# Kernel tuning notes

Hardware: AMD Instinct MI355X
Metric: run time of the kernel (lower is better)

## Reference

```python
import jax, jax.numpy as jnp
import numpy as np

N_ATOM = 10000
N_EDGE = 40000
D = 64          # fingerprint_dim
BOND_DIM = 10
EPS_BN = 1e-6
EPS_SM = 1e-8


def _bn(x, g, b, m, v):
    # BatchNorm1d in eval mode with running stats
    return (x - m) * jax.lax.rsqrt(v + EPS_BN) * g + b


def setup_inputs() -> dict:
    key = jax.random.key(0)
    ks = jax.random.split(key, 16)
    s = 0.05
    inp = {
        "atom": jax.random.normal(ks[0], (N_ATOM, D), jnp.float32),
        "bond_index": jax.random.randint(ks[1], (N_EDGE, 2), 0, N_ATOM, jnp.int64),
        "bond": jax.random.normal(ks[2], (N_EDGE, BOND_DIM), jnp.float32),
        # encoder: Linear(bond_dim, D*D) + BN(D*D)
        "enc_W": jax.random.normal(ks[3], (D * D, BOND_DIM), jnp.float32) * s,
        "enc_b": jnp.zeros((D * D,), jnp.float32),
        "bn1_g": jnp.ones((D * D,), jnp.float32),
        "bn1_b": jnp.zeros((D * D,), jnp.float32),
        "bn1_m": jnp.zeros((D * D,), jnp.float32),
        "bn1_v": jnp.ones((D * D,), jnp.float32),
        # align: Linear(2D, 1)
        "align_W": jax.random.normal(ks[4], (1, 2 * D), jnp.float32) * s,
        "align_b": jnp.zeros((1,), jnp.float32),
        # attend: Linear(D, D) + BN(D)
        "att_W": jax.random.normal(ks[5], (D, D), jnp.float32) * s,
        "att_b": jnp.zeros((D,), jnp.float32),
        "bn2_g": jnp.ones((D,), jnp.float32),
        "bn2_b": jnp.zeros((D,), jnp.float32),
        "bn2_m": jnp.zeros((D,), jnp.float32),
        "bn2_v": jnp.ones((D,), jnp.float32),
        # GRUCell(D, D)
        "gru_Wih": jax.random.normal(ks[6], (3 * D, D), jnp.float32) * s,
        "gru_Whh": jax.random.normal(ks[7], (3 * D, D), jnp.float32) * s,
        "gru_bih": jnp.zeros((3 * D,), jnp.float32),
        "gru_bhh": jnp.zeros((3 * D,), jnp.float32),
    }
    return inp


def reference(atom, bond_index, bond, enc_W, enc_b, bn1_g, bn1_b, bn1_m, bn1_v,
              align_W, align_b, att_W, att_b, bn2_g, bn2_b, bn2_m, bn2_v,
              gru_Wih, gru_Whh, gru_bih, gru_bhh):
    num_atom, atom_dim = atom.shape
    tgt = bond_index[:, 0]  # segment index (bond_index.t()[0])
    nbr = bond_index[:, 1]

    # encoder: Linear + BN + ReLU, then view as per-edge [D, D] matrices
    enc = jax.nn.relu(_bn(bond @ enc_W.T + enc_b, bn1_g, bn1_b, bn1_m, bn1_v))
    enc = enc.reshape(-1, atom_dim, atom_dim)            # [E, D, D]

    neighbor = jnp.einsum('ed,edf->ef', atom[nbr], enc)  # per-edge bmm [E, D]
    target_atom = atom[tgt]

    feat = jnp.concatenate([target_atom, neighbor], axis=-1)       # [E, 2D]
    align_score = jax.nn.leaky_relu(feat @ align_W.T + align_b)    # [E, 1]

    atend = _bn(neighbor @ att_W.T + att_b, bn2_g, bn2_b, bn2_m, bn2_v)  # [E, D]

    # segment softmax over edges grouped by target atom
    seg_max = jax.ops.segment_max(align_score, tgt, num_segments=num_atom)
    ex = jnp.exp(align_score - seg_max[tgt])
    denom = jax.ops.segment_sum(ex, tgt, num_segments=num_atom)[tgt] + EPS_SM
    w = ex / denom                                                   # [E, 1]

    context = jax.ops.segment_sum(w * atend, tgt, num_segments=num_atom)  # [N, D]
    context = jax.nn.elu(context)

    # GRUCell(context, atom)
    gi = context @ gru_Wih.T + gru_bih
    gh = atom @ gru_Whh.T + gru_bhh
    i_r, i_z, i_n = jnp.split(gi, 3, axis=-1)
    h_r, h_z, h_n = jnp.split(gh, 3, axis=-1)
    r = jax.nn.sigmoid(i_r + h_r)
    z = jax.nn.sigmoid(i_z + h_z)
    n = jnp.tanh(i_n + r * h_n)
    update = (1.0 - z) * n + z * atom
    return update
```

## Files before the change

kernel.cpp:

```cpp
#include <hip/hip_runtime.h>

#define N_ATOM 10000
#define N_EDGE 40000
#define DD 64
#define BOND_DIM 10
#define EPS_BN 1e-6f
#define EPS_SM 1e-8f
#define GA 8

typedef __attribute__((ext_vector_type(8))) short short8;
typedef __attribute__((ext_vector_type(2))) float float2v;
typedef __attribute__((ext_vector_type(4))) float float4v;
typedef __attribute__((ext_vector_type(16))) float float16v;
typedef unsigned int u32;

constexpr size_t OFF_AFRAG   = 0;
constexpr size_t OFF_ATTFRAG = 32768;
constexpr size_t OFF_ATTB    = 34816;
constexpr size_t OFF_WIHT    = 34880;
constexpr size_t OFF_WHHT    = 47168;
constexpr size_t OFF_DENOM   = 59456;
constexpr size_t OFF_CTX     = 69456;

__device__ __forceinline__ unsigned short f2bf(float x) {
    u32 u = __float_as_uint(x);
    u32 r = u + 0x7FFFu + ((u >> 16) & 1u);
    return (unsigned short)(r >> 16);
}

__global__ void fold_kernel(const float* enc_W, const float* enc_b,
                            const float* g1, const float* b1,
                            const float* m1, const float* v1,
                            const float* att_W, const float* att_b,
                            const float* g2, const float* b2v,
                            const float* m2, const float* v2,
                            const float* Wih, const float* Whh,
                            float* ws) {
    u32* wsu = (u32*)ws;
    size_t i = (size_t)blockIdx.x * 256 + threadIdx.x;
    if (i < 8192) {
        int d = i >> 7, rem = i & 127;
        int ch = rem >> 6, l = rem & 63;
        int c = d * 64 + ch * 32 + (l & 31);
        int kb = 8 * (l >> 5);
        float s = g1[c] * rsqrtf(v1[c] + EPS_BN);
        float bias = enc_b[c] * s + b1[c] - m1[c] * s;
        unsigned short h[8];
#pragma unroll
        for (int j = 0; j < 8; j++) {
            int k = kb + j;
            float v = (k < BOND_DIM) ? enc_W[c * BOND_DIM + k] * s
                                     : ((k == BOND_DIM) ? bias : 0.f);
            h[j] = f2bf(v);
        }
#pragma unroll
        for (int m = 0; m < 4; m++)
            wsu[OFF_AFRAG + i * 4 + m] = (u32)h[2 * m] | ((u32)h[2 * m + 1] << 16);
    } else if (i < 8704) {
        int idx = i - 8192;
        int l = idx & 63, fckh = idx >> 6;
        int fc = fckh >> 1, kh = fckh & 1, q = l >> 4;
        int n = (fc << 4) + (l & 15);
        float s = g2[n] * rsqrtf(v2[n] + EPS_BN);
        unsigned short h[8];
#pragma unroll
        for (int j = 0; j < 8; j++) {
            int k = 32 * kh + 8 * q + j;
            h[j] = f2bf(att_W[n * DD + k] * s);
        }
#pragma unroll
        for (int m = 0; m < 4; m++)
            wsu[OFF_ATTFRAG + (size_t)idx * 4 + m] = (u32)h[2 * m] | ((u32)h[2 * m + 1] << 16);
    } else if (i < 8768) {
        int f = i - 8704;
        float s = g2[f] * rsqrtf(v2[f] + EPS_BN);
        ws[OFF_ATTB + f] = att_b[f] * s + b2v[f] - m2[f] * s;
    } else if (i < 21056) {
        int j = i - 8768;
        int d = j / 192, t = j % 192;
        ws[OFF_WIHT + j] = Wih[t * DD + d];
    } else if (i < 33344) {
        int j = i - 21056;
        int d = j / 192, t = j % 192;
        ws[OFF_WHHT + j] = Whh[t * DD + d];
    } else {
        size_t z = i - 33344;
        if (z < (size_t)N_ATOM + (size_t)N_ATOM * DD) ws[OFF_DENOM + z] = 0.f;
    }
}

__global__ __launch_bounds__(256, 5) void edge_kernel(
    const float* atom, const int* bidx, const float* bond,
    const float* alignW, const float* alignb,
    const float* ws, float* denom, float* ctx) {
    __shared__ float s_bond[32][BOND_DIM];
    __shared__ float s_anbr[32][65];
    __shared__ float s_nbp[2][32][65];
    __shared__ float s_ex[32];
    __shared__ int   s_tgt[32];

    const int t = threadIdx.x;
    const int lane = t & 63;
    const int h = t >> 6;
    const int e0 = blockIdx.x * 32;

    for (int idx = t; idx < 32 * BOND_DIM; idx += 256)
        s_bond[idx / BOND_DIM][idx % BOND_DIM] = bond[(size_t)e0 * BOND_DIM + idx];
    if (t < 32) s_tgt[t] = bidx[2 * (e0 + t)];
    for (int e = h; e < 32; e += 4) {
        int nbr = bidx[2 * (e0 + e) + 1];
        s_anbr[e][lane] = atom[(size_t)nbr * DD + lane];
    }
    __syncthreads();

    const int eb = lane & 31;
    const int kb = 8 * (lane >> 5);
    short8 bfrag;
#pragma unroll
    for (int j = 0; j < 8; j++) {
        int k = kb + j;
        unsigned short hh = 0;
        if (k < BOND_DIM) hh = f2bf(s_bond[eb][k]);
        else if (k == BOND_DIM) hh = 0x3F80u;
        bfrag[j] = (short)hh;
    }

    const short8* afrag = (const short8*)((const u32*)ws + OFF_AFRAG);
    const float16v zero16 = {};
    const float2v zero2 = {0.f, 0.f};
    float2v nb0[8] = {}, nb1[8] = {};
    const int d0 = 16 * h;
    const int ph = blockIdx.x & 15;

#pragma unroll
    for (int it = 0; it < 16; it++) {
        int d = d0 + ((it + ph) & 15);
        short8 a0 = afrag[(size_t)(d * 2 + 0) * 64 + lane];
        short8 a1 = afrag[(size_t)(d * 2 + 1) * 64 + lane];
        float av = s_anbr[eb][d];
        float2v av2 = {av, av};
        float16v enc0 = __builtin_amdgcn_mfma_f32_32x32x16_bf16(a0, bfrag, zero16, 0, 0, 0);
        float16v enc1 = __builtin_amdgcn_mfma_f32_32x32x16_bf16(a1, bfrag, zero16, 0, 0, 0);
#pragma unroll
        for (int r = 0; r < 8; r++) {
            float2v e0v = {enc0[2 * r], enc0[2 * r + 1]};
            float2v e1v = {enc1[2 * r], enc1[2 * r + 1]};
            e0v = __builtin_elementwise_max(e0v, zero2);
            e1v = __builtin_elementwise_max(e1v, zero2);
            nb0[r] += av2 * e0v;
            nb1[r] += av2 * e1v;
        }
    }

    const int fro = 4 * (lane >> 5);
    if (h < 2) {
#pragma unroll
        for (int r = 0; r < 8; r++) {
            int e = 2 * r;
            int f = (e & 3) + 8 * (e >> 2) + fro;
            s_nbp[h][eb][f] = nb0[r].x;
            s_nbp[h][eb][f + 1] = nb0[r].y;
            s_nbp[h][eb][32 + f] = nb1[r].x;
            s_nbp[h][eb][32 + f + 1] = nb1[r].y;
        }
    }
    __syncthreads();
    if (h >= 2) {
#pragma unroll
        for (int r = 0; r < 8; r++) {
            int e = 2 * r;
            int f = (e & 3) + 8 * (e >> 2) + fro;
            s_nbp[h - 2][eb][f] += nb0[r].x;
            s_nbp[h - 2][eb][f + 1] += nb0[r].y;
            s_nbp[h - 2][eb][32 + f] += nb1[r].x;
            s_nbp[h - 2][eb][32 + f + 1] += nb1[r].y;
        }
    }
    __syncthreads();

    const int es = (h & 1) * 16;
    const int q = lane >> 4;
    const int r16 = lane & 15;
    float4v att[4];

    if (h < 2) {
        short8 na[2];
#pragma unroll
        for (int kh = 0; kh < 2; kh++)
#pragma unroll
            for (int j = 0; j < 8; j++) {
                int k = 32 * kh + 8 * q + j;
                na[kh][j] = (short)f2bf(s_nbp[0][es + r16][k] + s_nbp[1][es + r16][k]);
            }
        const short8* battfrag = (const short8*)((const u32*)ws + OFF_ATTFRAG);
        const float4v zero4 = {0.f, 0.f, 0.f, 0.f};
#pragma unroll
        for (int fc = 0; fc < 4; fc++) {
            att[fc] = __builtin_amdgcn_mfma_f32_16x16x32_bf16(na[0], battfrag[(fc * 2 + 0) * 64 + lane], zero4, 0, 0, 0);
            att[fc] = __builtin_amdgcn_mfma_f32_16x16x32_bf16(na[1], battfrag[(fc * 2 + 1) * 64 + lane], att[fc], 0, 0, 0);
            float ab = ws[OFF_ATTB + fc * 16 + r16];
#pragma unroll
            for (int r = 0; r < 4; r++) att[fc][r] += ab;
        }
    } else {
        const float aw1 = alignW[lane];
        const float aw2 = alignW[64 + lane];
        const float alb = alignb[0];
#pragma unroll 4
        for (int e = 0; e < 16; e++) {
            int le = es + e;
            int tgt = s_tgt[le];
            float nbv = s_nbp[0][le][lane] + s_nbp[1][le][lane];
            float v = atom[(size_t)tgt * DD + lane] * aw1 + nbv * aw2;
#pragma unroll
            for (int off = 32; off > 0; off >>= 1) v += __shfl_xor(v, off);
            float sc = v + alb;
            sc = sc > 0.f ? sc : 0.01f * sc;
            float ex = expf(sc);
            if (lane == 0) {
                s_ex[le] = ex;
                atomicAdd(&denom[tgt], ex);
            }
        }
    }
    __syncthreads();

    if (h < 2) {
#pragma unroll
        for (int r = 0; r < 4; r++) {
            int le = es + 4 * q + r;
            float exr = s_ex[le];
            int tg = s_tgt[le];
#pragma unroll
            for (int fc = 0; fc < 4; fc++)
                atomicAdd(&ctx[(size_t)tg * DD + fc * 16 + r16], exr * att[fc][r]);
        }
    }
}

__global__ __launch_bounds__(192) void gru_kernel(
    const float* atom, const float* ws, const float* denom, const float* ctx,
    const float* bih, const float* bhh, float* out) {
    __shared__ float sctx[GA][DD];
    __shared__ float satom[GA][DD];
    __shared__ float sgi[GA][192];
    __shared__ float sgh[GA][192];
    const int a0 = blockIdx.x * GA;
    const int t = threadIdx.x;

    for (int idx = t; idx < GA * DD; idx += 192) {
        int a = idx >> 6, f = idx & 63;
        float c = ctx[(size_t)(a0 + a) * DD + f] / (denom[a0 + a] + EPS_SM);
        sctx[a][f] = c > 0.f ? c : expm1f(c);
        satom[a][f] = atom[(size_t)(a0 + a) * DD + f];
    }
    __syncthreads();

    const float* wiht = ws + OFF_WIHT;
    const float* whht = ws + OFF_WHHT;
    float gi[GA], gh[GA];
    const float bi = bih[t], bh = bhh[t];
#pragma unroll
    for (int a = 0; a < GA; a++) { gi[a] = bi; gh[a] = bh; }
#pragma unroll 4
    for (int d = 0; d < DD; d++) {
        float wi = wiht[d * 192 + t];
        float wh = whht[d * 192 + t];
#pragma unroll
        for (int a = 0; a < GA; a++) {
            gi[a] = fmaf(wi, sctx[a][d], gi[a]);
            gh[a] = fmaf(wh, satom[a][d], gh[a]);
        }
    }
#pragma unroll
    for (int a = 0; a < GA; a++) { sgi[a][t] = gi[a]; sgh[a][t] = gh[a]; }
    __syncthreads();

    for (int idx = t; idx < GA * DD; idx += 192) {
        int a = idx >> 6, f = idx & 63;
        float r = 1.f / (1.f + expf(-(sgi[a][f] + sgh[a][f])));
        float z = 1.f / (1.f + expf(-(sgi[a][64 + f] + sgh[a][64 + f])));
        float n = tanhf(sgi[a][128 + f] + r * sgh[a][128 + f]);
        out[(size_t)(a0 + a) * DD + f] = (1.f - z) * n + z * satom[a][f];
    }
}

extern "C" void kernel_launch(void* const* d_in, const int* in_sizes, int n_in,
                              void* d_out, int out_size, void* d_ws, size_t ws_size,
                              hipStream_t stream) {
    const float* atom   = (const float*)d_in[0];
    const int*   bidx   = (const int*)d_in[1];
    const float* bond   = (const float*)d_in[2];
    const float* enc_W  = (const float*)d_in[3];
    const float* enc_b  = (const float*)d_in[4];
    const float* bn1_g  = (const float*)d_in[5];
    const float* bn1_b  = (const float*)d_in[6];
    const float* bn1_m  = (const float*)d_in[7];
    const float* bn1_v  = (const float*)d_in[8];
    const float* alignW = (const float*)d_in[9];
    const float* alignb = (const float*)d_in[10];
    const float* att_W  = (const float*)d_in[11];
    const float* att_b  = (const float*)d_in[12];
    const float* bn2_g  = (const float*)d_in[13];
    const float* bn2_b  = (const float*)d_in[14];
    const float* bn2_m  = (const float*)d_in[15];
    const float* bn2_v  = (const float*)d_in[16];
    const float* gWih   = (const float*)d_in[17];
    const float* gWhh   = (const float*)d_in[18];
    const float* gbih   = (const float*)d_in[19];
    const float* gbhh   = (const float*)d_in[20];

    float* ws  = (float*)d_ws;
    float* out = (float*)d_out;

    fold_kernel<<<2670, 256, 0, stream>>>(enc_W, enc_b, bn1_g, bn1_b, bn1_m, bn1_v,
                                          att_W, att_b, bn2_g, bn2_b, bn2_m, bn2_v,
                                          gWih, gWhh, ws);

    edge_kernel<<<N_EDGE / 32, 256, 0, stream>>>(
        atom, bidx, bond, alignW, alignb, ws,
        ws + OFF_DENOM, ws + OFF_CTX);

    gru_kernel<<<N_ATOM / GA, 192, 0, stream>>>(atom, ws, ws + OFF_DENOM, ws + OFF_CTX,
                                                gbih, gbhh, out);
}
```

Measured before the change: 147.5 us.

## Precompute per-atom target align score and drop rotated weight-fragment indexing

Adds a per-atom precomputation in the fold kernel of the target half of the align dot product (atom · alignW[:64]), stored in the workspace. The edge kernel then reads one scalar per edge instead of gathering a 64-float target atom row and doing the multiply. It also removes the per-block phase rotation of the d loop so weight fragment addresses become compile-time offsets, and lowers the edge kernel's min-blocks-per-SM launch bound from 5 to 4. The tradeoffs are extra fold-kernel work over all atoms, possibly more cache-bank contention on the shared weight fragments without the rotation, and occupancy changes from the relaxed bound.

```diff
diff --git a/kernel.cpp b/kernel.cpp
--- a/kernel.cpp
+++ b/kernel.cpp
@@ -19,8 +19,9 @@
 constexpr size_t OFF_ATTB    = 34816;
 constexpr size_t OFF_WIHT    = 34880;
 constexpr size_t OFF_WHHT    = 47168;
-constexpr size_t OFF_DENOM   = 59456;
-constexpr size_t OFF_CTX     = 69456;
+constexpr size_t OFF_SALIGN  = 59456;
+constexpr size_t OFF_DENOM   = 69456;
+constexpr size_t OFF_CTX     = 79456;
 
 __device__ __forceinline__ unsigned short f2bf(float x) {
     u32 u = __float_as_uint(x);
@@ -28,7 +29,8 @@
     return (unsigned short)(r >> 16);
 }
 
-__global__ void fold_kernel(const float* enc_W, const float* enc_b,
+__global__ void fold_kernel(const float* atom, const float* alignW,
+                            const float* enc_W, const float* enc_b,
                             const float* g1, const float* b1,
                             const float* m1, const float* v1,
                             const float* att_W, const float* att_b,
@@ -83,13 +85,24 @@
         int j = i - 21056;
         int d = j / 192, t = j % 192;
         ws[OFF_WHHT + j] = Whh[t * DD + d];
+    } else if (i < 43344) {
+        int a = i - 33344;
+        const float4* ar = (const float4*)(atom + (size_t)a * DD);
+        const float4* aw = (const float4*)alignW;
+        float s = 0.f;
+#pragma unroll
+        for (int qq = 0; qq < 16; qq++) {
+            float4 x = ar[qq], w = aw[qq];
+            s += x.x * w.x + x.y * w.y + x.z * w.z + x.w * w.w;
+        }
+        ws[OFF_SALIGN + a] = s;
     } else {
-        size_t z = i - 33344;
+        size_t z = i - 43344;
         if (z < (size_t)N_ATOM + (size_t)N_ATOM * DD) ws[OFF_DENOM + z] = 0.f;
     }
 }
 
-__global__ __launch_bounds__(256, 5) void edge_kernel(
+__global__ __launch_bounds__(256, 4) void edge_kernel(
     const float* atom, const int* bidx, const float* bond,
     const float* alignW, const float* alignb,
     const float* ws, float* denom, float* ctx) {
@@ -125,19 +138,17 @@
         bfrag[j] = (short)hh;
     }
 
-    const short8* afrag = (const short8*)((const u32*)ws + OFF_AFRAG);
+    const int d0 = 16 * h;
+    const short8* aw = (const short8*)((const u32*)ws + OFF_AFRAG) + ((size_t)(d0 * 2) * 64 + lane);
     const float16v zero16 = {};
     const float2v zero2 = {0.f, 0.f};
     float2v nb0[8] = {}, nb1[8] = {};
-    const int d0 = 16 * h;
-    const int ph = blockIdx.x & 15;
 
 #pragma unroll
     for (int it = 0; it < 16; it++) {
-        int d = d0 + ((it + ph) & 15);
-        short8 a0 = afrag[(size_t)(d * 2 + 0) * 64 + lane];
-        short8 a1 = afrag[(size_t)(d * 2 + 1) * 64 + lane];
-        float av = s_anbr[eb][d];
+        short8 a0 = aw[(size_t)(2 * it) * 64];
+        short8 a1 = aw[(size_t)(2 * it + 1) * 64];
+        float av = s_anbr[eb][d0 + it];
         float2v av2 = {av, av};
         float16v enc0 = __builtin_amdgcn_mfma_f32_32x32x16_bf16(a0, bfrag, zero16, 0, 0, 0);
         float16v enc1 = __builtin_amdgcn_mfma_f32_32x32x16_bf16(a1, bfrag, zero16, 0, 0, 0);
@@ -203,18 +214,17 @@
             for (int r = 0; r < 4; r++) att[fc][r] += ab;
         }
     } else {
-        const float aw1 = alignW[lane];
+        const float* salign = ws + OFF_SALIGN;
         const float aw2 = alignW[64 + lane];
         const float alb = alignb[0];
 #pragma unroll 4
         for (int e = 0; e < 16; e++) {
             int le = es + e;
             int tgt = s_tgt[le];
-            float nbv = s_nbp[0][le][lane] + s_nbp[1][le][lane];
-            float v = atom[(size_t)tgt * DD + lane] * aw1 + nbv * aw2;
+            float v = (s_nbp[0][le][lane] + s_nbp[1][le][lane]) * aw2;
 #pragma unroll
             for (int off = 32; off > 0; off >>= 1) v += __shfl_xor(v, off);
-            float sc = v + alb;
+            float sc = salign[tgt] + v + alb;
             sc = sc > 0.f ? sc : 0.01f * sc;
             float ex = expf(sc);
             if (lane == 0) {
@@ -313,7 +323,8 @@
     float* ws  = (float*)d_ws;
     float* out = (float*)d_out;
 
-    fold_kernel<<<2670, 256, 0, stream>>>(enc_W, enc_b, bn1_g, bn1_b, bn1_m, bn1_v,
+    fold_kernel<<<2709, 256, 0, stream>>>(atom, alignW,
+                                          enc_W, enc_b, bn1_g, bn1_b, bn1_m, bn1_v,
                                           att_W, att_b, bn2_g, bn2_b, bn2_m, bn2_v,
                                           gWih, gWhh, ws);
 
```

After: 155.6 us. +5.5%, slower.
